# Performance work log

Measured on AMD Instinct MI355X. Metric: run time of the kernel, lower is better.

Reference implementation:

```python
import jax, jax.numpy as jnp
import numpy as np

B, S, H = 4, 2048, 1024
I = 2816          # intermediate_size
E = 8             # num_experts
K = 2             # num_experts_per_token
AUX_COEF = 0.01


def setup_inputs() -> dict:
    key = jax.random.key(0)
    ks = jax.random.split(key, 5)
    scale = 0.02
    return {
        "hidden_states": jax.random.normal(ks[0], (B, S, H), dtype=jnp.float32),
        "gate_w": jax.random.normal(ks[1], (E, H), dtype=jnp.float32) * scale,   # router Linear weight [out=E, in=H]
        "Wg": jax.random.normal(ks[2], (E, I, H), dtype=jnp.float32) * scale,    # gate_proj weights
        "Wu": jax.random.normal(ks[3], (E, I, H), dtype=jnp.float32) * scale,    # up_proj weights
        "Wd": jax.random.normal(ks[4], (E, H, I), dtype=jnp.float32) * scale,    # down_proj weights
    }


def reference(hidden_states, gate_w, Wg, Wu, Wd):
    b, s, h = hidden_states.shape
    x = hidden_states.reshape(-1, h)                     # [T, H], T = b*s
    T = x.shape[0]

    # --- router (eval mode: no jitter noise) ---
    logits = jnp.einsum('th,eh->te', x, gate_w)          # [T, E]
    probs = jax.nn.softmax(logits, axis=-1)              # [T, E]
    w, idx = jax.lax.top_k(probs, K)                     # [T, K], [T, K]
    w = w / jnp.sum(w, axis=-1, keepdims=True)

    onehot = jax.nn.one_hot(idx, E, dtype=probs.dtype)   # [T, K, E]

    # --- auxiliary load-balancing loss (matches torch: mask summed over tokens, kept per-k) ---
    f_i = onehot.sum(axis=0) / T                         # [K, E]
    p_i = probs.mean(axis=0)                             # [E]
    aux_loss = E * jnp.sum(f_i * p_i) * AUX_COEF

    # per-token combine weight for each expert
    cw = jnp.einsum('tk,tke->te', w, onehot)             # [T, E]

    # --- expert SwiGLU FFNs, weighted combine (loop over fixed small E) ---
    out = jnp.zeros_like(x)
    for e in range(E):
        g = jax.nn.silu(x @ Wg[e].T)                     # [T, I]
        u = x @ Wu[e].T                                  # [T, I]
        out = out + cw[:, e:e + 1] * ((g * u) @ Wd[e].T) # [T, H]

    return out.reshape(b, s, h), aux_loss
```

## Files before the change

### kernel.cpp

```cpp
#include <hip/hip_runtime.h>

#define TT 8192
#define HD 1024
#define ID 2816
#define NE 8

typedef unsigned short u16;
typedef __attribute__((ext_vector_type(8))) __bf16 bf16x8;
typedef __attribute__((ext_vector_type(4))) float f32x4;

static constexpr int BM = 128;
static constexpr int BK = 64;
static constexpr int MAXSLOT = 17408;
static constexpr int MTILES  = 136;
static constexpr int NN1     = ID/BM;
static constexpr int G1      = MTILES*NN1;
static constexpr int G2      = MTILES*8*2;
static constexpr int RTR_BLK = 256;
static constexpr int RTR_CVT = 1024;
static constexpr int G1_CVT  = 512;

struct Meta {
  u16   zeros[32];
  int   cnt[NE];
  float psum[NE];
  int   cursor[NE];
  int   seg[12];
};

static constexpr size_t OFF_XH    = 0;
static constexpr size_t OFF_WGH   = OFF_XH   + (size_t)TT*HD*2;
static constexpr size_t OFF_WUH   = OFF_WGH  + (size_t)NE*ID*HD*2;
static constexpr size_t OFF_WDH   = OFF_WUH  + (size_t)NE*ID*HD*2;
static constexpr size_t OFF_ACT   = OFF_WDH  + (size_t)NE*HD*ID*2;
static constexpr size_t OFF_PERM  = OFF_ACT  + (size_t)MAXSLOT*ID*2;
static constexpr size_t OFF_TID   = OFF_PERM + (size_t)MAXSLOT*4;
static constexpr size_t OFF_TSLOT = OFF_TID  + (size_t)TT*2*4;
static constexpr size_t OFF_TW    = OFF_TSLOT+ (size_t)TT*2*4;
static constexpr size_t OFF_META  = OFF_TW   + (size_t)TT*2*4;
static constexpr size_t WS_NEED   = OFF_META + sizeof(Meta);
static constexpr size_t OFF_Y     = OFF_WGH;

__device__ __forceinline__ u16 f2bf(float f) {
  unsigned u = __float_as_uint(f);
  u += 0x7FFFu + ((u >> 16) & 1u);
  return (u16)(u >> 16);
}
__device__ __forceinline__ float bf2f(u16 h) {
  return __uint_as_float(((unsigned)h) << 16);
}

__device__ __forceinline__ float dot4(float4 a, float4 b) {
  return a.x*b.x + a.y*b.y + a.z*b.z + a.w*b.w;
}

__device__ __forceinline__ void gll16(const void* g, void* l) {
  __builtin_amdgcn_global_load_lds(
      (const __attribute__((address_space(1))) void*)g,
      (__attribute__((address_space(3))) void*)l, 16, 0, 0);
}

__device__ __forceinline__ void cvt8(const float* __restrict__ src, u16* __restrict__ dst) {
  const float4* s4 = (const float4*)src;
  float4 a = s4[0], b = s4[1];
  union { u16 h[8]; uint4 v; } r;
  r.h[0]=f2bf(a.x); r.h[1]=f2bf(a.y); r.h[2]=f2bf(a.z); r.h[3]=f2bf(a.w);
  r.h[4]=f2bf(b.x); r.h[5]=f2bf(b.y); r.h[6]=f2bf(b.z); r.h[7]=f2bf(b.w);
  *(uint4*)dst = r.v;
}

__global__ void k_init(int* __restrict__ perm, Meta* __restrict__ meta) {
  int gid  = blockIdx.x*blockDim.x + threadIdx.x;
  int nthr = gridDim.x*blockDim.x;
  for (int i = gid; i < MAXSLOT; i += nthr) perm[i] = -1;
  if (gid < 32) meta->zeros[gid] = 0;
  if (gid < NE) { meta->cnt[gid]=0; meta->psum[gid]=0.f; meta->cursor[gid]=0; }
}

__global__ void k_router(const float* __restrict__ x, const float* __restrict__ gw,
                         int* __restrict__ tke, float* __restrict__ tkw,
                         u16* __restrict__ xh, Meta* __restrict__ meta,
                         const float* __restrict__ Wg, const float* __restrict__ Wu,
                         u16* __restrict__ wgh) {
  if (blockIdx.x >= RTR_BLK) {
    const long per = (long)NE*ID*HD/8;
    long base = (long)(blockIdx.x - RTR_BLK)*256 + threadIdx.x;
    for (long idx = base; idx < 2*per; idx += (long)RTR_CVT*256) {
      const float* src = (idx < per) ? (Wg + idx*8) : (Wu + (idx-per)*8);
      cvt8(src, wgh + idx*8);
    }
    return;
  }
  __shared__ int   s_cnt[NE];
  __shared__ float s_ps[NE];
  int tid = threadIdx.x;
  if (tid < NE) { s_cnt[tid]=0; s_ps[tid]=0.f; }
  __syncthreads();
  int wv = tid>>6, ln = tid&63;
  for (int it = 0; it < 8; ++it) {
    int t = it*1024 + blockIdx.x*4 + wv;
    const float4* xp = (const float4*)(x + (size_t)t*HD + ln*16);
    float4 xv0=xp[0], xv1=xp[1], xv2=xp[2], xv3=xp[3];
    union { u16 h[8]; uint4 v; } r0, r1;
    r0.h[0]=f2bf(xv0.x); r0.h[1]=f2bf(xv0.y); r0.h[2]=f2bf(xv0.z); r0.h[3]=f2bf(xv0.w);
    r0.h[4]=f2bf(xv1.x); r0.h[5]=f2bf(xv1.y); r0.h[6]=f2bf(xv1.z); r0.h[7]=f2bf(xv1.w);
    r1.h[0]=f2bf(xv2.x); r1.h[1]=f2bf(xv2.y); r1.h[2]=f2bf(xv2.z); r1.h[3]=f2bf(xv2.w);
    r1.h[4]=f2bf(xv3.x); r1.h[5]=f2bf(xv3.y); r1.h[6]=f2bf(xv3.z); r1.h[7]=f2bf(xv3.w);
    uint4* xo = (uint4*)(xh + (size_t)t*HD + ln*16);
    xo[0] = r0.v; xo[1] = r1.v;
    float lg[NE];
    #pragma unroll
    for (int e=0;e<NE;++e) {
      const float4* gp = (const float4*)(gw + e*HD + ln*16);
      lg[e] = dot4(xv0,gp[0]) + dot4(xv1,gp[1]) + dot4(xv2,gp[2]) + dot4(xv3,gp[3]);
    }
    #pragma unroll
    for (int e=0;e<NE;++e) {
      #pragma unroll
      for (int off=32; off; off>>=1) lg[e] += __shfl_xor(lg[e], off);
    }
    if (ln == 0) {
      float mx = lg[0];
      #pragma unroll
      for (int e=1;e<NE;++e) mx = fmaxf(mx, lg[e]);
      float p[NE], s = 0.f;
      #pragma unroll
      for (int e=0;e<NE;++e) { p[e] = __expf(lg[e]-mx); s += p[e]; }
      float inv = 1.f/s;
      #pragma unroll
      for (int e=0;e<NE;++e) p[e] *= inv;
      int e1 = 0;
      #pragma unroll
      for (int e=1;e<NE;++e) if (p[e] > p[e1]) e1 = e;
      int e2 = (e1==0) ? 1 : 0;
      #pragma unroll
      for (int e=0;e<NE;++e) if (e!=e1 && p[e] > p[e2]) e2 = e;
      float ws2 = p[e1] + p[e2];
      tke[2*t]   = e1; tke[2*t+1] = e2;
      tkw[2*t]   = p[e1]/ws2; tkw[2*t+1] = p[e2]/ws2;
      atomicAdd(&s_cnt[e1], 1); atomicAdd(&s_cnt[e2], 1);
      #pragma unroll
      for (int e=0;e<NE;++e) atomicAdd(&s_ps[e], p[e]);
    }
  }
  __syncthreads();
  if (tid < NE) { atomicAdd(&meta->cnt[tid], s_cnt[tid]); atomicAdd(&meta->psum[tid], s_ps[tid]); }
}

__global__ void k_scan(Meta* __restrict__ meta, float* __restrict__ aux_out) {
  if (threadIdx.x == 0) {
    int s = 0;
    for (int e=0;e<NE;++e) { meta->seg[e] = s; s += ((meta->cnt[e]+BM-1)/BM)*BM; }
    meta->seg[NE] = s;
    float a = 0.f;
    for (int e=0;e<NE;++e)
      a += ((float)meta->cnt[e]/(float)TT) * (meta->psum[e]/(float)TT);
    aux_out[0] = (float)NE * 0.01f * a;
  }
}

__global__ void k_scatter(const int* __restrict__ tke,
                          Meta* __restrict__ meta, int* __restrict__ perm,
                          int* __restrict__ tslot) {
  int t = blockIdx.x*blockDim.x + threadIdx.x;
  if (t >= TT) return;
  for (int k=0;k<2;++k) {
    int e = tke[2*t+k];
    int pos = atomicAdd(&meta->cursor[e], 1);
    int slot = meta->seg[e] + pos;
    perm[slot]   = t;
    tslot[2*t+k] = slot;
  }
}


__launch_bounds__(256, 2)
__global__ void k_gemm1(const u16* __restrict__ xh, const u16* __restrict__ wgh, const u16* __restrict__ wuh,
                        const int* __restrict__ perm, const Meta* __restrict__ meta, u16* __restrict__ act,
                        const float* __restrict__ Wd, u16* __restrict__ wdh) {
  __shared__ u16 As[BM*BK], Gs[BM*BK], Us[BM*BK];
  int bid = blockIdx.x;
  if (bid >= G1) {
    const long per = (long)NE*ID*HD/8;
    long base = (long)(bid - G1)*256 + threadIdx.x;
    for (long idx = base; idx < per; idx += (long)G1_CVT*256)
      cvt8(Wd + idx*8, wdh + idx*8);
    return;
  }
  int wg  = (bid&7)*(G1/8) + (bid>>3);
  int band = wg/176, r = wg%176;
  int mt = band*8 + (r&7);
  int m0 = mt*BM;
  int n0 = (r>>3)*BM;
  int total = meta->seg[NE];
  if (m0 >= total) return;
  int e = 0;
  #pragma unroll
  for (int i=1;i<NE;++i) if (m0 >= meta->seg[i]) e = i;
  int tid = threadIdx.x;
  int srow = tid>>3;
  int scol = ((tid&7) ^ (srow&7)) * 8;
  const u16* zp = meta->zeros;
  int tok[4];
  const u16* ap[4]; const u16* gp[4]; const u16* up[4];
  #pragma unroll
  for (int j=0;j<4;++j) {
    tok[j] = perm[m0 + srow + 32*j];
    ap[j]  = xh + (size_t)(tok[j]<0?0:tok[j])*HD + scol;
    size_t rr = (size_t)e*ID + n0 + srow + 32*j;
    gp[j]  = wgh + rr*HD + scol;
    up[j]  = wuh + rr*HD + scol;
  }
  u16* lA = As + tid*8; u16* lG = Gs + tid*8; u16* lU = Us + tid*8;
  int wv = tid>>6, ln = tid&63;
  int wr = (wv>>1)*64, wc = (wv&1)*64;
  int lr = ln&15, kq = ln>>4;
  int kx = lr&7;
  f32x4 accg[4][4] = {};
  f32x4 accu[4][4] = {};
  for (int k0 = 0; k0 < HD; k0 += BK) {
    #pragma unroll
    for (int j=0;j<4;++j) {
      gll16(tok[j]<0 ? (const void*)zp : (const void*)(ap[j]+k0), lA + j*2048);
      gll16(gp[j]+k0, lG + j*2048);
      gll16(up[j]+k0, lU + j*2048);
    }
    __syncthreads();
    #pragma unroll
    for (int h=0; h<2; ++h) {
      int koff = ((h*4 + kq) ^ kx) * 8;
      bf16x8 af[4], gf[4], uf[4];
      #pragma unroll
      for (int m=0;m<4;++m) af[m] = *(const bf16x8*)&As[(wr+m*16+lr)*BK + koff];
      #pragma unroll
      for (int n=0;n<4;++n) {
        gf[n] = *(const bf16x8*)&Gs[(wc+n*16+lr)*BK + koff];
        uf[n] = *(const bf16x8*)&Us[(wc+n*16+lr)*BK + koff];
      }
      #pragma unroll
      for (int m=0;m<4;++m)
        #pragma unroll
        for (int n=0;n<4;++n) {
          accg[m][n] = __builtin_amdgcn_mfma_f32_16x16x32_bf16(af[m], gf[n], accg[m][n], 0,0,0);
          accu[m][n] = __builtin_amdgcn_mfma_f32_16x16x32_bf16(af[m], uf[n], accu[m][n], 0,0,0);
        }
    }
    __syncthreads();
  }
  int rb = wr + (ln>>4)*4;
  int cb = n0 + wc + (ln&15);
  #pragma unroll
  for (int m=0;m<4;++m)
    #pragma unroll
    for (int j=0;j<4;++j) {
      size_t row = (size_t)(m0 + rb + m*16 + j);
      u16* ap2 = act + row*ID + cb;
      #pragma unroll
      for (int n=0;n<4;++n) {
        float g = accg[m][n][j], u = accu[m][n][j];
        float sv = g / (1.f + __expf(-g));
        ap2[n*16] = f2bf(sv*u);
      }
    }
}

__launch_bounds__(256, 3)
__global__ void k_gemm2(const u16* __restrict__ act, const u16* __restrict__ wdh,
                        const Meta* __restrict__ meta, u16* __restrict__ y) {
  __shared__ u16 As[BM*BK], Bs[BM*BK];
  int bid = blockIdx.x;
  int wg  = (bid&7)*(G2/8) + (bid>>3);
  int kh  = (wg >= G2/2) ? 1 : 0;
  int w2  = wg - kh*(G2/2);
  int band = w2>>6, r = w2&63;
  int mt = band*8 + (r&7);
  int m0 = mt*BM;
  int n0 = (r>>3)*BM;
  int total = meta->seg[NE];
  if (m0 >= total) return;
  int e = 0;
  #pragma unroll
  for (int i=1;i<NE;++i) if (m0 >= meta->seg[i]) e = i;
  int kbase = kh * (ID/2);
  u16* yh = y + (size_t)kh*MAXSLOT*HD;
  int tid = threadIdx.x;
  int srow = tid>>3;
  int scol = ((tid&7) ^ (srow&7)) * 8;
  const u16* ab = act + (size_t)(m0 + srow)*ID + kbase + scol;
  const u16* b0 = wdh + ((size_t)e*HD + n0 + srow)*ID + kbase + scol;
  u16* lA = As + tid*8; u16* lB = Bs + tid*8;
  int wv = tid>>6, ln = tid&63;
  int wr = (wv>>1)*64, wc = (wv&1)*64;
  int lr = ln&15, kq = ln>>4;
  int kx = lr&7;
  f32x4 acc[4][4] = {};
  for (int k0 = 0; k0 < ID/2; k0 += BK) {
    #pragma unroll
    for (int j=0;j<4;++j) {
      gll16(ab + (size_t)j*32*ID + k0, lA + j*2048);
      gll16(b0 + (size_t)j*32*ID + k0, lB + j*2048);
    }
    __syncthreads();
    #pragma unroll
    for (int h=0; h<2; ++h) {
      int koff = ((h*4 + kq) ^ kx) * 8;
      bf16x8 af[4], bf[4];
      #pragma unroll
      for (int m=0;m<4;++m) af[m] = *(const bf16x8*)&As[(wr+m*16+lr)*BK + koff];
      #pragma unroll
      for (int n=0;n<4;++n) bf[n] = *(const bf16x8*)&Bs[(wc+n*16+lr)*BK + koff];
      #pragma unroll
      for (int m=0;m<4;++m)
        #pragma unroll
        for (int n=0;n<4;++n)
          acc[m][n] = __builtin_amdgcn_mfma_f32_16x16x32_bf16(af[m], bf[n], acc[m][n], 0,0,0);
    }
    __syncthreads();
  }
  int rb = wr + (ln>>4)*4;
  int cb = n0 + wc + (ln&15);
  #pragma unroll
  for (int m=0;m<4;++m)
    #pragma unroll
    for (int j=0;j<4;++j) {
      u16* yp = yh + (size_t)(m0 + rb + m*16 + j)*HD + cb;
      #pragma unroll
      for (int n=0;n<4;++n) yp[n*16] = f2bf(acc[m][n][j]);
    }
}

__global__ void k_combine(const u16* __restrict__ y, const int* __restrict__ tslot,
                          const float* __restrict__ tkw, float* __restrict__ out) {
  int idx = blockIdx.x*blockDim.x + threadIdx.x;
  int t = idx >> 7;
  int c = (idx & 127) * 8;
  int s0 = tslot[2*t], s1 = tslot[2*t+1];
  float w0 = tkw[2*t], w1 = tkw[2*t+1];
  const size_t H2 = (size_t)MAXSLOT*HD;
  union { uint4 v; u16 h[8]; } a0, a1, b0, b1;
  a0.v = *(const uint4*)(y + (size_t)s0*HD + c);
  a1.v = *(const uint4*)(y + H2 + (size_t)s0*HD + c);
  b0.v = *(const uint4*)(y + (size_t)s1*HD + c);
  b1.v = *(const uint4*)(y + H2 + (size_t)s1*HD + c);
  float r[8];
  #pragma unroll
  for (int i=0;i<8;++i)
    r[i] = w0*(bf2f(a0.h[i]) + bf2f(a1.h[i])) + w1*(bf2f(b0.h[i]) + bf2f(b1.h[i]));
  float4 o0 = {r[0],r[1],r[2],r[3]}, o1 = {r[4],r[5],r[6],r[7]};
  float4* op = (float4*)(out + (size_t)t*HD + c);
  op[0] = o0; op[1] = o1;
}

extern "C" void kernel_launch(void* const* d_in, const int* in_sizes, int n_in,
                              void* d_out, int out_size, void* d_ws, size_t ws_size,
                              hipStream_t stream) {
  if (ws_size < WS_NEED) return;
  const float* x  = (const float*)d_in[0];
  const float* gw = (const float*)d_in[1];
  const float* Wg = (const float*)d_in[2];
  const float* Wu = (const float*)d_in[3];
  const float* Wd = (const float*)d_in[4];
  float* out = (float*)d_out;
  char* ws = (char*)d_ws;
  u16* xh   = (u16*)(ws + OFF_XH);
  u16* wgh  = (u16*)(ws + OFF_WGH);
  u16* wdh  = (u16*)(ws + OFF_WDH);
  u16* act  = (u16*)(ws + OFF_ACT);
  int* perm = (int*)(ws + OFF_PERM);
  int* tke  = (int*)(ws + OFF_TID);
  int* tslot= (int*)(ws + OFF_TSLOT);
  float* tkw= (float*)(ws + OFF_TW);
  Meta* meta= (Meta*)(ws + OFF_META);
  u16* y    = (u16*)(ws + OFF_Y);
  u16* wuh  = (u16*)(ws + OFF_WUH);

  k_init   <<<128, 256, 0, stream>>>(perm, meta);
  k_router <<<RTR_BLK + RTR_CVT, 256, 0, stream>>>(x, gw, tke, tkw, xh, meta, Wg, Wu, wgh);
  k_scan   <<<1, 64, 0, stream>>>(meta, out + (size_t)TT*HD);
  k_scatter<<<32, 256, 0, stream>>>(tke, meta, perm, tslot);
  k_gemm1  <<<G1 + G1_CVT, 256, 0, stream>>>(xh, wgh, wuh, perm, meta, act, Wd, wdh);
  k_gemm2  <<<G2, 256, 0, stream>>>(act, wdh, meta, y);
  k_combine<<<TT*HD/8/256, 256, 0, stream>>>(y, tslot, tkw, out);
}
```

Before: 568.8 us.

## Move Wg/Wu conversion to init, fold scan into scatter, interleave Wd conversion blocks

The Wg/Wu fp32-to-bf16 conversion blocks move from the router launch into k_init, and k_scan is folded into k_scatter, where each thread recomputes the segment offsets. This removes one launch and separates the router's work from the conversion traffic. In gemm1 the Wd conversion blocks are now interleaved among the GEMM blocks (every eighth group) rather than appended at the end of the grid, so the conversion overlaps with compute. The block-to-tile remap adds some idle blocks and changes scheduling order, which could hurt cache locality.

After: 565.9 us. About the same (-0.5%).

```diff
diff --git a/kernel.cpp b/kernel.cpp
--- a/kernel.cpp
+++ b/kernel.cpp
@@ -15,10 +15,12 @@
 static constexpr int MTILES  = 136;
 static constexpr int NN1     = ID/BM;
 static constexpr int G1      = MTILES*NN1;
+static constexpr int G1GRP   = 428;
+static constexpr int G1T     = G1GRP*8;
+static constexpr int CVT1N   = 53*8;
 static constexpr int G2      = MTILES*8*2;
-static constexpr int RTR_BLK = 256;
-static constexpr int RTR_CVT = 1024;
-static constexpr int G1_CVT  = 512;
+static constexpr int INIT_BLK= 128;
+static constexpr int INIT_CVT= 1024;
 
 struct Meta {
   u16   zeros[32];
@@ -69,9 +71,28 @@
   *(uint4*)dst = r.v;
 }
 
-__global__ void k_init(int* __restrict__ perm, Meta* __restrict__ meta) {
-  int gid  = blockIdx.x*blockDim.x + threadIdx.x;
-  int nthr = gridDim.x*blockDim.x;
+__device__ __forceinline__ void calc_seg(const Meta* meta, int* seg) {
+  int s = 0;
+  #pragma unroll
+  for (int e=0;e<NE;++e) { seg[e] = s; s += ((meta->cnt[e]+BM-1)/BM)*BM; }
+  seg[NE] = s;
+}
+
+__global__ void k_init(int* __restrict__ perm, Meta* __restrict__ meta,
+                       const float* __restrict__ Wg, const float* __restrict__ Wu,
+                       u16* __restrict__ wgh) {
+  int bid = blockIdx.x, tid = threadIdx.x;
+  if (bid >= INIT_BLK) {
+    const long per = (long)NE*ID*HD/8;
+    long base = (long)(bid - INIT_BLK)*256 + tid;
+    for (long idx = base; idx < 2*per; idx += (long)INIT_CVT*256) {
+      const float* src = (idx < per) ? (Wg + idx*8) : (Wu + (idx-per)*8);
+      cvt8(src, wgh + idx*8);
+    }
+    return;
+  }
+  int gid  = bid*256 + tid;
+  int nthr = INIT_BLK*256;
   for (int i = gid; i < MAXSLOT; i += nthr) perm[i] = -1;
   if (gid < 32) meta->zeros[gid] = 0;
   if (gid < NE) { meta->cnt[gid]=0; meta->psum[gid]=0.f; meta->cursor[gid]=0; }
@@ -79,18 +100,7 @@
 
 __global__ void k_router(const float* __restrict__ x, const float* __restrict__ gw,
                          int* __restrict__ tke, float* __restrict__ tkw,
-                         u16* __restrict__ xh, Meta* __restrict__ meta,
-                         const float* __restrict__ Wg, const float* __restrict__ Wu,
-                         u16* __restrict__ wgh) {
-  if (blockIdx.x >= RTR_BLK) {
-    const long per = (long)NE*ID*HD/8;
-    long base = (long)(blockIdx.x - RTR_BLK)*256 + threadIdx.x;
-    for (long idx = base; idx < 2*per; idx += (long)RTR_CVT*256) {
-      const float* src = (idx < per) ? (Wg + idx*8) : (Wu + (idx-per)*8);
-      cvt8(src, wgh + idx*8);
-    }
-    return;
-  }
+                         u16* __restrict__ xh, Meta* __restrict__ meta) {
   __shared__ int   s_cnt[NE];
   __shared__ float s_ps[NE];
   int tid = threadIdx.x;
@@ -147,27 +157,26 @@
   if (tid < NE) { atomicAdd(&meta->cnt[tid], s_cnt[tid]); atomicAdd(&meta->psum[tid], s_ps[tid]); }
 }
 
-__global__ void k_scan(Meta* __restrict__ meta, float* __restrict__ aux_out) {
-  if (threadIdx.x == 0) {
-    int s = 0;
-    for (int e=0;e<NE;++e) { meta->seg[e] = s; s += ((meta->cnt[e]+BM-1)/BM)*BM; }
-    meta->seg[NE] = s;
+__global__ void k_scatter(const int* __restrict__ tke,
+                          Meta* __restrict__ meta, int* __restrict__ perm,
+                          int* __restrict__ tslot, float* __restrict__ aux_out) {
+  int seg[NE+1];
+  calc_seg(meta, seg);
+  if (blockIdx.x == 0 && threadIdx.x == 0) {
+    #pragma unroll
+    for (int e=0;e<=NE;++e) meta->seg[e] = seg[e];
     float a = 0.f;
+    #pragma unroll
     for (int e=0;e<NE;++e)
       a += ((float)meta->cnt[e]/(float)TT) * (meta->psum[e]/(float)TT);
     aux_out[0] = (float)NE * 0.01f * a;
   }
-}
-
-__global__ void k_scatter(const int* __restrict__ tke,
-                          Meta* __restrict__ meta, int* __restrict__ perm,
-                          int* __restrict__ tslot) {
   int t = blockIdx.x*blockDim.x + threadIdx.x;
   if (t >= TT) return;
   for (int k=0;k<2;++k) {
     int e = tke[2*t+k];
     int pos = atomicAdd(&meta->cursor[e], 1);
-    int slot = meta->seg[e] + pos;
+    int slot = seg[e] + pos;
     perm[slot]   = t;
     tslot[2*t+k] = slot;
   }
@@ -180,14 +189,17 @@
                         const float* __restrict__ Wd, u16* __restrict__ wdh) {
   __shared__ u16 As[BM*BK], Gs[BM*BK], Us[BM*BK];
   int bid = blockIdx.x;
-  if (bid >= G1) {
+  int g = bid >> 3, l = bid & 7;
+  if ((g & 7) == 7) {
     const long per = (long)NE*ID*HD/8;
-    long base = (long)(bid - G1)*256 + threadIdx.x;
-    for (long idx = base; idx < per; idx += (long)G1_CVT*256)
+    long base = (long)((g>>3)*8 + l)*256 + threadIdx.x;
+    for (long idx = base; idx < per; idx += (long)CVT1N*256)
       cvt8(Wd + idx*8, wdh + idx*8);
     return;
   }
-  int wg  = (bid&7)*(G1/8) + (bid>>3);
+  int gg = g - ((g+1) >> 3);
+  int wg = l*375 + gg;
+  if (wg >= G1) return;
   int band = wg/176, r = wg%176;
   int mt = band*8 + (r&7);
   int m0 = mt*BM;
@@ -257,8 +269,8 @@
       u16* ap2 = act + row*ID + cb;
       #pragma unroll
       for (int n=0;n<4;++n) {
-        float g = accg[m][n][j], u = accu[m][n][j];
-        float sv = g / (1.f + __expf(-g));
+        float g2 = accg[m][n][j], u = accu[m][n][j];
+        float sv = g2 / (1.f + __expf(-g2));
         ap2[n*16] = f2bf(sv*u);
       }
     }
@@ -364,6 +376,7 @@
   char* ws = (char*)d_ws;
   u16* xh   = (u16*)(ws + OFF_XH);
   u16* wgh  = (u16*)(ws + OFF_WGH);
+  u16* wuh  = (u16*)(ws + OFF_WUH);
   u16* wdh  = (u16*)(ws + OFF_WDH);
   u16* act  = (u16*)(ws + OFF_ACT);
   int* perm = (int*)(ws + OFF_PERM);
@@ -372,13 +385,11 @@
   float* tkw= (float*)(ws + OFF_TW);
   Meta* meta= (Meta*)(ws + OFF_META);
   u16* y    = (u16*)(ws + OFF_Y);
-  u16* wuh  = (u16*)(ws + OFF_WUH);
-
-  k_init   <<<128, 256, 0, stream>>>(perm, meta);
-  k_router <<<RTR_BLK + RTR_CVT, 256, 0, stream>>>(x, gw, tke, tkw, xh, meta, Wg, Wu, wgh);
-  k_scan   <<<1, 64, 0, stream>>>(meta, out + (size_t)TT*HD);
-  k_scatter<<<32, 256, 0, stream>>>(tke, meta, perm, tslot);
-  k_gemm1  <<<G1 + G1_CVT, 256, 0, stream>>>(xh, wgh, wuh, perm, meta, act, Wd, wdh);
+
+  k_init   <<<INIT_BLK + INIT_CVT, 256, 0, stream>>>(perm, meta, Wg, Wu, wgh);
+  k_router <<<256, 256, 0, stream>>>(x, gw, tke, tkw, xh, meta);
+  k_scatter<<<32, 256, 0, stream>>>(tke, meta, perm, tslot, out + (size_t)TT*HD);
+  k_gemm1  <<<G1T, 256, 0, stream>>>(xh, wgh, wuh, perm, meta, act, Wd, wdh);
   k_gemm2  <<<G2, 256, 0, stream>>>(act, wdh, meta, y);
   k_combine<<<TT*HD/8/256, 256, 0, stream>>>(y, tslot, tkw, out);
 }
```
